# Performance work log

Measured on AMD Instinct MI355X. Metric: run time of the kernel, lower is better.

The kernel has to match this reference:

```python
import jax, jax.numpy as jnp
import numpy as np

B, IN, H = 16384, 10, 1024
GD_ITERS, GD_LR = 7, 0.001


def setup_inputs() -> dict:
    key = jax.random.key(0)
    ks = jax.random.split(key, 16)
    s_in = 1.0 / np.sqrt(IN)
    s_h = 1.0 / np.sqrt(H)
    inp = {
        'x': jax.random.normal(ks[0], (B, IN), jnp.float32),
        'hidden': jax.random.normal(ks[1], (B, H), jnp.float32),
        'c': jax.random.normal(ks[2], (B, H), jnp.float32),
        'mid_price': jax.random.normal(ks[3], (B,), jnp.float32),
        # nn.Linear weights are [out, in]; biases [out]
        'Wf_w': jax.random.uniform(ks[4], (H, IN), jnp.float32, -s_in, s_in),
        'Wf_b': jax.random.uniform(ks[5], (H,), jnp.float32, -s_in, s_in),
        'Uf_w': jax.random.uniform(ks[6], (H, H), jnp.float32, -s_h, s_h),
        'Wi_w': jax.random.uniform(ks[7], (H, IN), jnp.float32, -s_in, s_in),
        'Wi_b': jax.random.uniform(ks[8], (H,), jnp.float32, -s_in, s_in),
        'Ui_w': jax.random.uniform(ks[9], (H, H), jnp.float32, -s_h, s_h),
        'Wc_w': jax.random.uniform(ks[10], (H, IN), jnp.float32, -s_in, s_in),
        'Wc_b': jax.random.uniform(ks[11], (H,), jnp.float32, -s_in, s_in),
        'Uc_w': jax.random.uniform(ks[12], (H, H), jnp.float32, -s_h, s_h),
        'Wo_w': jax.random.uniform(ks[13], (H, IN), jnp.float32, -s_in, s_in),
        'Wo_b': jax.random.uniform(ks[14], (H,), jnp.float32, -s_in, s_in),
        'Uo_w': jax.random.uniform(ks[15], (H, H), jnp.float32, -s_h, s_h),
    }
    return inp


def reference(x, hidden, c, mid_price, Wf_w, Wf_b, Uf_w, Wi_w, Wi_b, Ui_w,
              Wc_w, Wc_b, Uc_w, Wo_w, Wo_b, Uo_w):
    mp = mid_price.reshape(-1, 1)                       # [B,1]
    f_t = jax.nn.sigmoid(x @ Wf_w.T + Wf_b + hidden @ Uf_w.T)
    i_t = jax.nn.sigmoid(x @ Wi_w.T + Wi_b + hidden @ Ui_w.T)
    c_tilda = jnp.tanh(x @ Wc_w.T + Wc_b + hidden @ Uc_w.T)
    o_t = jax.nn.sigmoid(x @ Wo_w.T + Wo_b + hidden @ Uo_w.T)
    c_new = f_t * c + i_t * c_tilda
    h_std = o_t * jnp.tanh(c_new)
    r_t = jnp.concatenate([f_t, i_t, c_tilda, o_t, c_new, h_std], axis=1)  # [B,6H]

    bsz = r_t.shape[0]
    theta = jnp.zeros((6 * H, 1), dtype=r_t.dtype)

    def gd_step(_, th):
        err = r_t @ th - mp                             # [B,1]
        grad = 2.0 * (r_t.T @ err) / bsz                # [6H,1]
        return th - GD_LR * grad

    theta = jax.lax.fori_loop(0, GD_ITERS, gd_step, theta)

    importance = jnp.mean(jnp.abs(theta.reshape(6, H)), axis=1)  # [6]
    max_idx = jnp.argmax(importance)
    h_new = jax.lax.dynamic_slice(r_t, (0, max_idx * H), (bsz, H))
    return (h_new, c_new)
```

## Files before the change

### kernel.cpp

```cpp
#include <hip/hip_runtime.h>
#include <cstdint>
#include <cstddef>

#define Bsz   16384
#define INsz  10
#define Hsz   1024
#define N4    4096
#define NK    34
#define SIXH  6144
#define GDI   7
#define LR    0.001f
#define NPART 512

typedef _Float16 f16;
typedef __attribute__((ext_vector_type(8))) _Float16 f16x8;
typedef __attribute__((ext_vector_type(4))) _Float16 f16x4;
typedef __attribute__((ext_vector_type(4))) float    f32x4;

__device__ __forceinline__ void llds16(const f16* g, f16* l) {
    __builtin_amdgcn_global_load_lds(
        (__attribute__((address_space(1))) void*)(uintptr_t)g,
        (__attribute__((address_space(3))) void*)(uintptr_t)l,
        16, 0, 0);
}

__device__ __forceinline__ float sigm(float z)   { return 1.f / (1.f + __expf(-z)); }
__device__ __forceinline__ float tanh_f(float z) { return 1.f - 2.f / (__expf(2.f * z) + 1.f); }


__global__ void k_prepA(const float* __restrict__ hid, const float* __restrict__ x,
                        f16* __restrict__ A2) {
    int c = blockIdx.x * 256 + threadIdx.x;
    int mt  = c / 17408;
    int rem = c - mt * 17408;
    int ks  = rem >> 9;
    int rb  = (rem >> 6) & 7;
    int l   = rem & 63;
    int row = mt * 128 + rb * 16 + (l & 15);
    int k0  = ks * 32 + (l >> 4) * 8;
    f16x8 v;
    if (k0 + 8 <= Hsz) {
        float4 t0 = *(const float4*)&hid[(size_t)row * Hsz + k0];
        float4 t1 = *(const float4*)&hid[(size_t)row * Hsz + k0 + 4];
        v[0]=(f16)t0.x; v[1]=(f16)t0.y; v[2]=(f16)t0.z; v[3]=(f16)t0.w;
        v[4]=(f16)t1.x; v[5]=(f16)t1.y; v[6]=(f16)t1.z; v[7]=(f16)t1.w;
    } else {
#pragma unroll
        for (int e = 0; e < 8; ++e) {
            int k = k0 + e;
            float f = 0.f;
            if (k < Hsz + INsz)       f = x[(size_t)row * INsz + (k - Hsz)];
            else if (k == Hsz + INsz) f = 1.0f;
            v[e] = (f16)f;
        }
    }
    *(f16x8*)&A2[(size_t)c * 8] = v;
}

__global__ void k_prepU(const float* __restrict__ Uf, const float* __restrict__ Ui,
                        const float* __restrict__ Uc, const float* __restrict__ Uo,
                        const float* __restrict__ Wf, const float* __restrict__ Wi,
                        const float* __restrict__ Wc, const float* __restrict__ Wo,
                        const float* __restrict__ bf_, const float* __restrict__ bi_,
                        const float* __restrict__ bc_, const float* __restrict__ bo_,
                        f16* __restrict__ U2) {
    int c = blockIdx.x * 256 + threadIdx.x;
    int nt  = c / 17408;
    int rem = c - nt * 17408;
    int ks  = rem >> 9;
    int rb  = (rem >> 6) & 7;
    int l   = rem & 63;
    int cc  = rb * 16 + (l & 15);
    int g   = cc >> 5;
    int h   = nt * 32 + (cc & 31);
    int k0  = ks * 32 + (l >> 4) * 8;
    const float* U = (g == 0) ? Uf : (g == 1) ? Ui : (g == 2) ? Uc : Uo;
    f16x8 v;
    if (k0 + 8 <= Hsz) {
        float4 t0 = *(const float4*)&U[(size_t)h * Hsz + k0];
        float4 t1 = *(const float4*)&U[(size_t)h * Hsz + k0 + 4];
        v[0]=(f16)t0.x; v[1]=(f16)t0.y; v[2]=(f16)t0.z; v[3]=(f16)t0.w;
        v[4]=(f16)t1.x; v[5]=(f16)t1.y; v[6]=(f16)t1.z; v[7]=(f16)t1.w;
    } else {
        const float* W  = (g == 0) ? Wf  : (g == 1) ? Wi  : (g == 2) ? Wc  : Wo;
        const float* Bb = (g == 0) ? bf_ : (g == 1) ? bi_ : (g == 2) ? bc_ : bo_;
#pragma unroll
        for (int e = 0; e < 8; ++e) {
            int k = k0 + e;
            float f = 0.f;
            if (k < Hsz + INsz)       f = W[h * INsz + (k - Hsz)];
            else if (k == Hsz + INsz) f = Bb[h];
            v[e] = (f16)f;
        }
    }
    *(f16x8*)&U2[(size_t)c * 8] = v;
}

__global__ void k_zero(float* __restrict__ p, int n) {
    int i = blockIdx.x * 256 + threadIdx.x;
    if (i < n) p[i] = 0.f;
}

#define IMG(r, cidx) ((r) * 128 + ((cidx) ^ (((r) & 15) << 3)))

__global__ __launch_bounds__(256, 3) void k_gemm(const f16* __restrict__ A2,
                                                 const f16* __restrict__ U2,
                                                 const float* __restrict__ c_in,
                                                 f16* __restrict__ rt4,
                                                 float* __restrict__ c_out) {
    __shared__ __align__(16) f16 sm[3 * 8192];
    const int bid = blockIdx.x;
    const int swz = ((bid & 7) << 9) | (bid >> 3);
    const int bm = swz >> 5, bn = swz & 31;
    const int tid = threadIdx.x, wave = tid >> 6, lane = tid & 63;
    const int wr = wave >> 1, wc = wave & 1;
    const int r = lane & 15, q = lane >> 4;

    const f16* gA = A2 + (size_t)bm * (NK * 4096);
    const f16* gB = U2 + (size_t)bn * (NK * 4096);

    auto stage = [&](int ks) {
        f16* s = &sm[(ks % 3) * 8192];
        const f16* a = gA + (size_t)ks * 4096;
        const f16* b = gB + (size_t)ks * 4096;
        llds16(a + tid * 8,        &s[tid * 8]);
        llds16(a + 2048 + tid * 8, &s[2048 + tid * 8]);
        llds16(b + tid * 8,        &s[4096 + tid * 8]);
        llds16(b + 2048 + tid * 8, &s[6144 + tid * 8]);
    };

    f32x4 acc[4][4];
#pragma unroll
    for (int i = 0; i < 4; ++i)
#pragma unroll
        for (int j = 0; j < 4; ++j) acc[i][j] = (f32x4){0.f, 0.f, 0.f, 0.f};

    stage(0); stage(1);

    for (int ks = 0; ks < NK; ++ks) {
        if (ks + 2 < NK) {
            stage(ks + 2);
            asm volatile("s_waitcnt vmcnt(8)" ::: "memory");
        } else if (ks + 1 < NK) {
            asm volatile("s_waitcnt vmcnt(4)" ::: "memory");
        } else {
            asm volatile("s_waitcnt vmcnt(0)" ::: "memory");
        }
        __builtin_amdgcn_s_barrier();
        __builtin_amdgcn_sched_barrier(0);
        const f16* s = &sm[(ks % 3) * 8192];
        f16x8 af[4], bf[4];
#pragma unroll
        for (int i = 0; i < 4; ++i)
            af[i] = *(const f16x8*)&s[(wr * 4 + i) * 512 + lane * 8];
#pragma unroll
        for (int j = 0; j < 4; ++j)
            bf[j] = *(const f16x8*)&s[4096 + (wc * 4 + j) * 512 + lane * 8];
        asm volatile("s_waitcnt lgkmcnt(0)" ::: "memory");
        __builtin_amdgcn_sched_barrier(0);
        __builtin_amdgcn_s_barrier();
#pragma unroll
        for (int i = 0; i < 4; ++i)
#pragma unroll
            for (int j = 0; j < 4; ++j)
                acc[i][j] = __builtin_amdgcn_mfma_f32_16x16x32_f16(af[i], bf[j], acc[i][j], 0, 0, 0);
    }

    f16* img = sm;
#pragma unroll
    for (int i = 0; i < 4; ++i)
#pragma unroll
        for (int j = 0; j < 4; ++j)
#pragma unroll
            for (int reg = 0; reg < 4; ++reg) {
                int row_l = wr * 64 + i * 16 + q * 4 + reg;
                int col_l = wc * 64 + j * 16 + r;
                img[IMG(row_l, col_l)] = (f16)acc[i][j][reg];
            }
    asm volatile("s_waitcnt lgkmcnt(0)" ::: "memory");
    __builtin_amdgcn_s_barrier();
    __builtin_amdgcn_sched_barrier(0);

    const int bcol = bn * 32;
#pragma unroll
    for (int s_ = 0; s_ < 2; ++s_) {
        int a  = s_ * 256 + tid;
        int row = a >> 2, ho = (a & 3) * 8;
        int grow = bm * 128 + row;
        f16x8 pf = *(const f16x8*)&img[IMG(row,      ho)];
        f16x8 pi = *(const f16x8*)&img[IMG(row, 32 + ho)];
        f16x8 pc = *(const f16x8*)&img[IMG(row, 64 + ho)];
        f16x8 po = *(const f16x8*)&img[IMG(row, 96 + ho)];
        float4 c0 = *(const float4*)&c_in[(size_t)grow * Hsz + bcol + ho];
        float4 c1 = *(const float4*)&c_in[(size_t)grow * Hsz + bcol + ho + 4];
        float cv[8] = {c0.x, c0.y, c0.z, c0.w, c1.x, c1.y, c1.z, c1.w};
        f16x8 of, oi, oc, oo;
        float cn[8];
#pragma unroll
        for (int e = 0; e < 8; ++e) {
            float f  = sigm((float)pf[e]);
            float i_ = sigm((float)pi[e]);
            float ct = tanh_f((float)pc[e]);
            float o  = sigm((float)po[e]);
            cn[e] = f * cv[e] + i_ * ct;
            of[e] = (f16)f; oi[e] = (f16)i_; oc[e] = (f16)ct; oo[e] = (f16)o;
        }
        size_t rb_ = (size_t)grow * N4 + bcol + ho;
        *(f16x8*)&rt4[rb_]        = of;
        *(f16x8*)&rt4[rb_ + 1024] = oi;
        *(f16x8*)&rt4[rb_ + 2048] = oc;
        *(f16x8*)&rt4[rb_ + 3072] = oo;
        *(float4*)&c_out[(size_t)grow * Hsz + bcol + ho]     = (float4){cn[0], cn[1], cn[2], cn[3]};
        *(float4*)&c_out[(size_t)grow * Hsz + bcol + ho + 4] = (float4){cn[4], cn[5], cn[6], cn[7]};
    }
}

__global__ __launch_bounds__(256) void k_gd(const f16* __restrict__ rt4,
                                            const float* __restrict__ cn,
                                            const float* __restrict__ mp,
                                            const float* __restrict__ theta,
                                            float* __restrict__ part) {
    const int tid = threadIdx.x;
    const int r0 = blockIdx.x * 32;
    const int wave = tid >> 6, lane = tid & 63;

    float thA[8], thB[8], thC[4], thD[4];
    float grA[8] = {0}, grB[8] = {0}, grC[4] = {0}, grD[4] = {0};
#pragma unroll
    for (int k = 0; k < 8; ++k) {
        thA[k] = theta[tid * 8 + k];
        thB[k] = theta[2048 + tid * 8 + k];
    }
#pragma unroll
    for (int k = 0; k < 4; ++k) {
        thC[k] = theta[4096 + tid * 4 + k];
        thD[k] = theta[5120 + tid * 4 + k];
    }

    __shared__ float red[16];

    for (int rb = 0; rb < 32; rb += 4) {
        f16x8 dA[4], dB[4];
        f32x4 dC[4];
        float hs[4][4];
        float s[4];
#pragma unroll
        for (int rr = 0; rr < 4; ++rr) {
            const size_t row = (size_t)(r0 + rb + rr);
            dA[rr] = *(const f16x8*)&rt4[row * N4 + tid * 8];
            dB[rr] = *(const f16x8*)&rt4[row * N4 + 2048 + tid * 8];
            dC[rr] = *(const f32x4*)&cn[row * Hsz + tid * 4];
            f16x4 dO = *(const f16x4*)&rt4[row * N4 + 3072 + tid * 4];
            float a = 0.f;
#pragma unroll
            for (int k = 0; k < 8; ++k) a += (float)dA[rr][k] * thA[k];
#pragma unroll
            for (int k = 0; k < 8; ++k) a += (float)dB[rr][k] * thB[k];
#pragma unroll
            for (int k = 0; k < 4; ++k) {
                float h = (float)dO[k] * tanh_f(dC[rr][k]);
                hs[rr][k] = h;
                a += dC[rr][k] * thC[k] + h * thD[k];
            }
            s[rr] = a;
        }
#pragma unroll
        for (int rr = 0; rr < 4; ++rr)
#pragma unroll
            for (int off = 32; off > 0; off >>= 1)
                s[rr] += __shfl_xor(s[rr], off, 64);
        if (lane == 0) {
#pragma unroll
            for (int rr = 0; rr < 4; ++rr) red[rr * 4 + wave] = s[rr];
        }
        __syncthreads();
        float e[4];
#pragma unroll
        for (int rr = 0; rr < 4; ++rr)
            e[rr] = (red[rr * 4 + 0] + red[rr * 4 + 1] + red[rr * 4 + 2] + red[rr * 4 + 3])
                    - mp[r0 + rb + rr];
        __syncthreads();
#pragma unroll
        for (int rr = 0; rr < 4; ++rr) {
#pragma unroll
            for (int k = 0; k < 8; ++k) {
                grA[k] += e[rr] * (float)dA[rr][k];
                grB[k] += e[rr] * (float)dB[rr][k];
            }
#pragma unroll
            for (int k = 0; k < 4; ++k) {
                grC[k] += e[rr] * dC[rr][k];
                grD[k] += e[rr] * hs[rr][k];
            }
        }
    }

    float* pb = &part[(size_t)blockIdx.x * SIXH];
#pragma unroll
    for (int k = 0; k < 8; ++k) {
        pb[tid * 8 + k]        = grA[k];
        pb[2048 + tid * 8 + k] = grB[k];
    }
#pragma unroll
    for (int k = 0; k < 4; ++k) {
        pb[4096 + tid * 4 + k] = grC[k];
        pb[5120 + tid * 4 + k] = grD[k];
    }
}

__global__ void k_reduce(const float* __restrict__ part, float* __restrict__ theta) {
    __shared__ float sred[256];
    const int tid = threadIdx.x;
    const int c = (tid & 31) + blockIdx.x * 32;
    const int pl = tid >> 5;
    float s = 0.f;
    for (int p = pl; p < NPART; p += 8) s += part[(size_t)p * SIXH + c];
    sred[tid] = s;
    __syncthreads();
    if (pl == 0) {
        float acc = s;
#pragma unroll
        for (int k = 1; k < 8; ++k) acc += sred[k * 32 + (tid & 31)];
        theta[c] -= (2.f * LR / (float)Bsz) * acc;
    }
}

__global__ void k_argmax(const float* __restrict__ theta, float* __restrict__ outc) {
    __shared__ float w[6][4];
    const int tid = threadIdx.x;
    const int wave = tid >> 6, lane = tid & 63;
    for (int g = 0; g < 6; ++g) {
        float s = 0.f;
        for (int j = tid; j < 1024; j += 256) s += fabsf(theta[g * 1024 + j]);
#pragma unroll
        for (int off = 32; off > 0; off >>= 1) s += __shfl_xor(s, off, 64);
        if (lane == 0) w[g][wave] = s;
    }
    __syncthreads();
    if (tid == 0) {
        int best = 0;
        float bv = w[0][0] + w[0][1] + w[0][2] + w[0][3];
        for (int g = 1; g < 6; ++g) {
            float v = w[g][0] + w[g][1] + w[g][2] + w[g][3];
            if (v > bv) { bv = v; best = g; }
        }
        outc[0] = (float)best;
    }
}

__global__ void k_gather(const f16* __restrict__ rt4, const float* __restrict__ cnp,
                         float* __restrict__ outh) {
    const int idx = (int)cnp[0];
    int t = blockIdx.x * 256 + threadIdx.x;
    int b = t >> 8, h4 = (t & 255) * 4;
    float* o = &outh[(size_t)b * Hsz + h4];
    if (idx < 4) {
        f16x4 v = *(const f16x4*)&rt4[(size_t)b * N4 + idx * 1024 + h4];
#pragma unroll
        for (int k = 0; k < 4; ++k) o[k] = (float)v[k];
    } else if (idx == 4) {
        f32x4 v = *(const f32x4*)&cnp[(size_t)b * Hsz + h4];
#pragma unroll
        for (int k = 0; k < 4; ++k) o[k] = v[k];
    } else {
        f16x4 ov = *(const f16x4*)&rt4[(size_t)b * N4 + 3072 + h4];
        f32x4 cv = *(const f32x4*)&cnp[(size_t)b * Hsz + h4];
#pragma unroll
        for (int k = 0; k < 4; ++k) o[k] = (float)ov[k] * tanh_f(cv[k]);
    }
}

__global__ void k_fix(const f16* __restrict__ rt4, const float* __restrict__ c_in,
                      float* __restrict__ out) {
    if (threadIdx.x == 0 && blockIdx.x == 0) {
        int idx = (int)out[(size_t)Bsz * Hsz];
        float f  = (float)rt4[0];
        float i_ = (float)rt4[1024];
        float ct = (float)rt4[2048];
        float o  = (float)rt4[3072];
        float cn = f * c_in[0] + i_ * ct;
        out[(size_t)Bsz * Hsz] = cn;
        if (idx == 4)      out[0] = cn;
        else if (idx == 5) out[0] = o * tanh_f(cn);
    }
}

extern "C" void kernel_launch(void* const* d_in, const int* in_sizes, int n_in,
                              void* d_out, int out_size, void* d_ws, size_t ws_size,
                              hipStream_t stream) {
    const float* x    = (const float*)d_in[0];
    const float* hid  = (const float*)d_in[1];
    const float* c    = (const float*)d_in[2];
    const float* mp   = (const float*)d_in[3];
    const float* Wf_w = (const float*)d_in[4];
    const float* Wf_b = (const float*)d_in[5];
    const float* Uf_w = (const float*)d_in[6];
    const float* Wi_w = (const float*)d_in[7];
    const float* Wi_b = (const float*)d_in[8];
    const float* Ui_w = (const float*)d_in[9];
    const float* Wc_w = (const float*)d_in[10];
    const float* Wc_b = (const float*)d_in[11];
    const float* Uc_w = (const float*)d_in[12];
    const float* Wo_w = (const float*)d_in[13];
    const float* Wo_b = (const float*)d_in[14];
    const float* Uo_w = (const float*)d_in[15];
    float* out  = (float*)d_out;
    float* outc = out + (size_t)Bsz * Hsz;

    f16* rt4 = (f16*)d_ws;
    uint8_t* oh = (uint8_t*)d_out;
    f16*   U2    = (f16*)oh;
    f16*   A2    = (f16*)(oh + 8912896);
    float* theta = (float*)(oh + 44564480);
    float* part  = (float*)(oh + 44589056);

    k_prepU<<<2176, 256, 0, stream>>>(Uf_w, Ui_w, Uc_w, Uo_w,
                                      Wf_w, Wi_w, Wc_w, Wo_w,
                                      Wf_b, Wi_b, Wc_b, Wo_b, U2);
    k_prepA<<<8704, 256, 0, stream>>>(hid, x, A2);
    k_gemm<<<4096, 256, 0, stream>>>(A2, U2, c, rt4, outc);
    k_zero<<<24, 256, 0, stream>>>(theta, SIXH);
    for (int it = 0; it < GDI; ++it) {
        k_gd<<<NPART, 256, 0, stream>>>(rt4, outc, mp, theta, part);
        k_reduce<<<SIXH / 32, 256, 0, stream>>>(part, theta);
    }
    k_argmax<<<1, 256, 0, stream>>>(theta, outc);
    k_gather<<<(Bsz * Hsz / 4) / 256, 256, 0, stream>>>(rt4, outc, out);
    k_fix<<<1, 64, 0, stream>>>(rt4, c, out);
}
```

Before: 866.9 us.

## Double gradient partitions and remap k_gd threads to per-gate 4-column slices

The gradient-descent kernel now launches 1024 blocks of 16 rows each instead of 512 blocks of 32 rows, with a 4-blocks-per-CU launch bound. Each thread now owns 4 columns of every gate, loaded as f16x4 and stored as f32x4, and each sync step handles 2 rows instead of 4. The partial-gradient buffer moves to the start of the output scratch area so it can hold the doubled partition count, and the reduce loop is unrolled. The aim is more memory-level parallelism in the bandwidth-bound GD sweeps. The cost is twice as much partial data for k_reduce to read, narrower vector loads, and more barriers per row.

```diff
diff --git a/kernel.cpp b/kernel.cpp
--- a/kernel.cpp
+++ b/kernel.cpp
@@ -10,7 +10,8 @@
 #define SIXH  6144
 #define GDI   7
 #define LR    0.001f
-#define NPART 512
+#define NPART 1024
+#define RPB   (Bsz / NPART)
 
 typedef _Float16 f16;
 typedef __attribute__((ext_vector_type(8))) _Float16 f16x8;
@@ -215,78 +216,76 @@
     }
 }
 
-__global__ __launch_bounds__(256) void k_gd(const f16* __restrict__ rt4,
-                                            const float* __restrict__ cn,
-                                            const float* __restrict__ mp,
-                                            const float* __restrict__ theta,
-                                            float* __restrict__ part) {
+__global__ __launch_bounds__(256, 4) void k_gd(const f16* __restrict__ rt4,
+                                               const float* __restrict__ cn,
+                                               const float* __restrict__ mp,
+                                               const float* __restrict__ theta,
+                                               float* __restrict__ part) {
     const int tid = threadIdx.x;
-    const int r0 = blockIdx.x * 32;
+    const int r0 = blockIdx.x * RPB;
     const int wave = tid >> 6, lane = tid & 63;
-
-    float thA[8], thB[8], thC[4], thD[4];
-    float grA[8] = {0}, grB[8] = {0}, grC[4] = {0}, grD[4] = {0};
-#pragma unroll
-    for (int k = 0; k < 8; ++k) {
-        thA[k] = theta[tid * 8 + k];
-        thB[k] = theta[2048 + tid * 8 + k];
-    }
-#pragma unroll
-    for (int k = 0; k < 4; ++k) {
-        thC[k] = theta[4096 + tid * 4 + k];
-        thD[k] = theta[5120 + tid * 4 + k];
-    }
-
-    __shared__ float red[16];
-
-    for (int rb = 0; rb < 32; rb += 4) {
-        f16x8 dA[4], dB[4];
-        f32x4 dC[4];
-        float hs[4][4];
-        float s[4];
-#pragma unroll
-        for (int rr = 0; rr < 4; ++rr) {
+    const int c4 = tid * 4;
+
+    f32x4 thG[4], thC, thD;
+    f32x4 grG[4], grC, grD;
+#pragma unroll
+    for (int g = 0; g < 4; ++g) {
+        thG[g] = *(const f32x4*)&theta[g * 1024 + c4];
+        grG[g] = (f32x4){0.f, 0.f, 0.f, 0.f};
+    }
+    thC = *(const f32x4*)&theta[4096 + c4];
+    thD = *(const f32x4*)&theta[5120 + c4];
+    grC = (f32x4){0.f, 0.f, 0.f, 0.f};
+    grD = (f32x4){0.f, 0.f, 0.f, 0.f};
+
+    __shared__ float red[8];
+
+    for (int rb = 0; rb < RPB; rb += 2) {
+        f16x4 dG[2][4];
+        f32x4 dC[2], hs[2];
+        float s[2];
+#pragma unroll
+        for (int rr = 0; rr < 2; ++rr) {
             const size_t row = (size_t)(r0 + rb + rr);
-            dA[rr] = *(const f16x8*)&rt4[row * N4 + tid * 8];
-            dB[rr] = *(const f16x8*)&rt4[row * N4 + 2048 + tid * 8];
-            dC[rr] = *(const f32x4*)&cn[row * Hsz + tid * 4];
-            f16x4 dO = *(const f16x4*)&rt4[row * N4 + 3072 + tid * 4];
+#pragma unroll
+            for (int g = 0; g < 4; ++g)
+                dG[rr][g] = *(const f16x4*)&rt4[row * N4 + g * 1024 + c4];
+            dC[rr] = *(const f32x4*)&cn[row * Hsz + c4];
             float a = 0.f;
 #pragma unroll
-            for (int k = 0; k < 8; ++k) a += (float)dA[rr][k] * thA[k];
-#pragma unroll
-            for (int k = 0; k < 8; ++k) a += (float)dB[rr][k] * thB[k];
+            for (int g = 0; g < 4; ++g)
+#pragma unroll
+                for (int k = 0; k < 4; ++k) a += (float)dG[rr][g][k] * thG[g][k];
 #pragma unroll
             for (int k = 0; k < 4; ++k) {
-                float h = (float)dO[k] * tanh_f(dC[rr][k]);
+                float h = (float)dG[rr][3][k] * tanh_f(dC[rr][k]);
                 hs[rr][k] = h;
                 a += dC[rr][k] * thC[k] + h * thD[k];
             }
             s[rr] = a;
         }
 #pragma unroll
-        for (int rr = 0; rr < 4; ++rr)
+        for (int rr = 0; rr < 2; ++rr)
 #pragma unroll
             for (int off = 32; off > 0; off >>= 1)
                 s[rr] += __shfl_xor(s[rr], off, 64);
         if (lane == 0) {
-#pragma unroll
-            for (int rr = 0; rr < 4; ++rr) red[rr * 4 + wave] = s[rr];
+            red[wave]     = s[0];
+            red[4 + wave] = s[1];
         }
         __syncthreads();
-        float e[4];
-#pragma unroll
-        for (int rr = 0; rr < 4; ++rr)
+        float e[2];
+#pragma unroll
+        for (int rr = 0; rr < 2; ++rr)
             e[rr] = (red[rr * 4 + 0] + red[rr * 4 + 1] + red[rr * 4 + 2] + red[rr * 4 + 3])
                     - mp[r0 + rb + rr];
         __syncthreads();
 #pragma unroll
-        for (int rr = 0; rr < 4; ++rr) {
-#pragma unroll
-            for (int k = 0; k < 8; ++k) {
-                grA[k] += e[rr] * (float)dA[rr][k];
-                grB[k] += e[rr] * (float)dB[rr][k];
-            }
+        for (int rr = 0; rr < 2; ++rr) {
+#pragma unroll
+            for (int g = 0; g < 4; ++g)
+#pragma unroll
+                for (int k = 0; k < 4; ++k) grG[g][k] += e[rr] * (float)dG[rr][g][k];
 #pragma unroll
             for (int k = 0; k < 4; ++k) {
                 grC[k] += e[rr] * dC[rr][k];
@@ -297,15 +296,9 @@
 
     float* pb = &part[(size_t)blockIdx.x * SIXH];
 #pragma unroll
-    for (int k = 0; k < 8; ++k) {
-        pb[tid * 8 + k]        = grA[k];
-        pb[2048 + tid * 8 + k] = grB[k];
-    }
-#pragma unroll
-    for (int k = 0; k < 4; ++k) {
-        pb[4096 + tid * 4 + k] = grC[k];
-        pb[5120 + tid * 4 + k] = grD[k];
-    }
+    for (int g = 0; g < 4; ++g) *(f32x4*)&pb[g * 1024 + c4] = grG[g];
+    *(f32x4*)&pb[4096 + c4] = grC;
+    *(f32x4*)&pb[5120 + c4] = grD;
 }
 
 __global__ void k_reduce(const float* __restrict__ part, float* __restrict__ theta) {
@@ -314,6 +307,7 @@
     const int c = (tid & 31) + blockIdx.x * 32;
     const int pl = tid >> 5;
     float s = 0.f;
+#pragma unroll 4
     for (int p = pl; p < NPART; p += 8) s += part[(size_t)p * SIXH + c];
     sred[tid] = s;
     __syncthreads();
@@ -411,8 +405,8 @@
     uint8_t* oh = (uint8_t*)d_out;
     f16*   U2    = (f16*)oh;
     f16*   A2    = (f16*)(oh + 8912896);
-    float* theta = (float*)(oh + 44564480);
-    float* part  = (float*)(oh + 44589056);
+    float* part  = (float*)oh;
+    float* theta = (float*)(oh + 25165824);
 
     k_prepU<<<2176, 256, 0, stream>>>(Uf_w, Ui_w, Uc_w, Uo_w,
                                       Wf_w, Wi_w, Wc_w, Wo_w,
```

Result: faster. 778.8 us (-10.2%).
